# Optimization experiments

Measured on AMD Instinct MI355X. Metric: run time of the kernel, lower is better.

The kernel has to match this reference:

```python
import jax, jax.numpy as jnp
import numpy as np

N = 500000
C = 128
V = 65536


def setup_inputs() -> dict:
    key = jax.random.key(0)
    k1, k2, k3, k4 = jax.random.split(key, 4)
    feats = jax.random.normal(k1, (N, C), dtype=jnp.float32)
    W1 = jax.random.normal(k2, (C, C), dtype=jnp.float32) * (1.0 / np.sqrt(C))
    b1 = jnp.zeros((C,), dtype=jnp.float32)
    W2 = jax.random.normal(k3, (C, C), dtype=jnp.float32) * (1.0 / np.sqrt(C))
    b2 = jnp.zeros((C,), dtype=jnp.float32)
    idx = jax.random.randint(k4, (N,), 0, V, dtype=jnp.int32)
    return {"feats": feats, "W1": W1, "b1": b1, "W2": W2, "b2": b2,
            "idx": idx, "num_voxels": V}


def reference(feats, W1, b1, W2, b2, idx, num_voxels):
    # AvgPooling: per-voxel mean of point features (spvoxelize with counts)
    counts = jax.ops.segment_sum(jnp.ones((feats.shape[0],), feats.dtype), idx,
                                 num_segments=num_voxels)  # [V]
    pooled = jax.ops.segment_sum(feats, idx, num_segments=num_voxels)  # [V, C]
    pooled = pooled / jnp.clip(counts, 1.0)[:, None]
    # Upsample (nearest=True): each point gathers its voxel's pooled feature
    up = pooled[idx]  # [N, C]
    # os = x - Upsample(vs, x); os.F = mlp(os.F) * x.F; os.F = mlp2(os.F)
    os = feats - up
    h = jax.nn.relu(os @ W1 + b1) * feats
    out = jax.nn.relu(h @ W2 + b2)
    return out
```

## Files before the change

kernel.cpp:

```cpp
#include <hip/hip_runtime.h>
#include <hip/hip_fp16.h>

typedef _Float16 f16;
typedef _Float16 f16x8 __attribute__((ext_vector_type(8)));
typedef float f32x4 __attribute__((ext_vector_type(4)));

constexpr int C = 128;
constexpr int V = 65536;
constexpr int PTS = 64;
constexpr int BLOCK = 256;
constexpr int BKT = 64;

union U16 { uint4 u; f16x8 h; };

__global__ void zero_cnt(int4* __restrict__ cnt) {
    const int t = blockIdx.x * blockDim.x + threadIdx.x;
    cnt[t] = make_int4(0, 0, 0, 0);
}

__global__ void bucket_scatter(const int* __restrict__ idx, int* __restrict__ cnt,
                               int* __restrict__ bucket, int n) {
    const int t = blockIdx.x * blockDim.x + threadIdx.x;
    if (t < n) {
        const int v = idx[t];
        const int slot = atomicAdd(&cnt[v], 1);
        if (slot < BKT) bucket[(v << 6) + slot] = t;
    }
}

__global__ void __launch_bounds__(256)
pool_bucket(const float* __restrict__ feats, const int* __restrict__ bucket,
            const int* __restrict__ cnt, __half* __restrict__ pooled) {
    const int v = blockIdx.x * 4 + (threadIdx.x >> 6);
    const int lane = threadIdx.x & 63;
    const int e = min(cnt[v], BKT);
    const int* b = bucket + (v << 6);
    float ax = 0.f, ay = 0.f, bx = 0.f, by = 0.f;
    float cx = 0.f, cy = 0.f, dx = 0.f, dy = 0.f;
    int j = 0;
    for (; j + 4 <= e; j += 4) {
        const int p0 = b[j], p1 = b[j + 1], p2 = b[j + 2], p3 = b[j + 3];
        const float2 f0 = *reinterpret_cast<const float2*>(feats + (size_t)p0 * C + lane * 2);
        const float2 f1 = *reinterpret_cast<const float2*>(feats + (size_t)p1 * C + lane * 2);
        const float2 f2 = *reinterpret_cast<const float2*>(feats + (size_t)p2 * C + lane * 2);
        const float2 f3 = *reinterpret_cast<const float2*>(feats + (size_t)p3 * C + lane * 2);
        ax += f0.x; ay += f0.y; bx += f1.x; by += f1.y;
        cx += f2.x; cy += f2.y; dx += f3.x; dy += f3.y;
    }
    for (; j < e; ++j) {
        const int p0 = b[j];
        const float2 f0 = *reinterpret_cast<const float2*>(feats + (size_t)p0 * C + lane * 2);
        ax += f0.x; ay += f0.y;
    }
    const float rc = e ? 1.0f / (float)e : 0.f;
    *reinterpret_cast<__half2*>(pooled + (size_t)v * C + lane * 2) =
        __floats2half2_rn((ax + bx + cx + dx) * rc, (ay + by + cy + dy) * rc);
}

__global__ void __launch_bounds__(BLOCK)
mlp_mfma(const float* __restrict__ feats,
         const float* __restrict__ W1g,
         const float* __restrict__ b1g,
         const float* __restrict__ W2g,
         const float* __restrict__ b2g,
         const int* __restrict__ idx,
         const __half* __restrict__ pooled,
         float* __restrict__ out,
         int n) {
    __shared__ f16 osh_lds[PTS * C];
    __shared__ f16 f_lds[PTS * C];

    const int t = threadIdx.x;
    const int lane = t & 63;
    const int wv = t >> 6;
    const int l15 = lane & 15;
    const int lg = lane >> 4;
    const int chBase = 32 * wv;

    const int ch0 = chBase + l15;
    const int ch1 = chBase + 16 + l15;
    f16x8 w1f[2][4], w2f[2][4];
#pragma unroll
    for (int m = 0; m < 2; ++m) {
        const int ch = (m == 0) ? ch0 : ch1;
#pragma unroll
        for (int s = 0; s < 4; ++s) {
            f16x8 a, b;
#pragma unroll
            for (int j = 0; j < 8; ++j) {
                const int k = s * 32 + lg * 8 + j;
                a[j] = (f16)W1g[k * C + ch];
                b[j] = (f16)W2g[k * C + ch];
            }
            w1f[m][s] = a;
            w2f[m][s] = b;
        }
    }
    const float b1v[2] = {b1g[ch0], b1g[ch1]};
    const float b2v[2] = {b2g[ch0], b2g[ch1]};

    const int sp = t >> 2;
    const int sc = (t & 3) * 32;

    for (long long base = (long long)blockIdx.x * PTS; base < n;
         base += (long long)gridDim.x * PTS) {
        {
            const long long p = base + sp;
            union { float4 v[8]; float f[32]; } ff;
            union { uint4 u[4]; __half h[32]; } pl;
            if (p < n) {
#pragma unroll
                for (int j = 0; j < 8; ++j)
                    ff.v[j] = *reinterpret_cast<const float4*>(feats + (size_t)p * C + sc + j * 4);
                const int v = idx[p];
                const uint4* pp = reinterpret_cast<const uint4*>(pooled + (size_t)v * C + sc);
#pragma unroll
                for (int j = 0; j < 4; ++j) pl.u[j] = pp[j];
            } else {
#pragma unroll
                for (int j = 0; j < 8; ++j) ff.v[j] = make_float4(0.f, 0.f, 0.f, 0.f);
#pragma unroll
                for (int j = 0; j < 4; ++j) pl.u[j] = make_uint4(0, 0, 0, 0);
            }
            union { uint4 u[4]; f16 h[32]; } osv, fvh;
#pragma unroll
            for (int j = 0; j < 32; ++j) {
                const float fj = ff.f[j];
                const float mj = __half2float(pl.h[j]);
                osv.h[j] = (f16)(fj - mj);
                fvh.h[j] = (f16)fj;
            }
#pragma unroll
            for (int u = 0; u < 4; ++u) {
                const int byte = (sp * 256 + (sc + u * 8) * 2) ^ ((sp & 7) << 4);
                *reinterpret_cast<uint4*>(reinterpret_cast<char*>(osh_lds) + byte) = osv.u[u];
                *reinterpret_cast<uint4*>(reinterpret_cast<char*>(f_lds) + byte) = fvh.u[u];
            }
        }
        __syncthreads();

        f32x4 acc[2][4];
#pragma unroll
        for (int m = 0; m < 2; ++m)
#pragma unroll
            for (int q = 0; q < 4; ++q)
                acc[m][q] = (f32x4){b1v[m], b1v[m], b1v[m], b1v[m]};

#pragma unroll
        for (int s = 0; s < 4; ++s) {
            f16x8 af[4];
#pragma unroll
            for (int q = 0; q < 4; ++q) {
                const int p = q * 16 + l15;
                const int byte = (p * 256 + (s * 32 + lg * 8) * 2) ^ ((p & 7) << 4);
                U16 tmp;
                tmp.u = *reinterpret_cast<const uint4*>(reinterpret_cast<const char*>(osh_lds) + byte);
                af[q] = tmp.h;
            }
#pragma unroll
            for (int m = 0; m < 2; ++m)
#pragma unroll
                for (int q = 0; q < 4; ++q)
                    acc[m][q] = __builtin_amdgcn_mfma_f32_16x16x32_f16(af[q], w1f[m][s], acc[m][q], 0, 0, 0);
        }
        __syncthreads();

#pragma unroll
        for (int m = 0; m < 2; ++m) {
            const int ch = chBase + m * 16 + l15;
#pragma unroll
            for (int q = 0; q < 4; ++q)
#pragma unroll
                for (int r = 0; r < 4; ++r) {
                    const int d = q * 16 + lg * 4 + r;
                    const int byte = (d * 256 + ch * 2) ^ ((d & 7) << 4);
                    const float fval = (float)*reinterpret_cast<const f16*>(
                        reinterpret_cast<const char*>(f_lds) + byte);
                    const float hv = fmaxf(acc[m][q][r], 0.f) * fval;
                    *reinterpret_cast<f16*>(reinterpret_cast<char*>(osh_lds) + byte) = (f16)hv;
                }
        }
        __syncthreads();

        f32x4 acc2[2][4];
#pragma unroll
        for (int m = 0; m < 2; ++m)
#pragma unroll
            for (int q = 0; q < 4; ++q)
                acc2[m][q] = (f32x4){b2v[m], b2v[m], b2v[m], b2v[m]};

#pragma unroll
        for (int s = 0; s < 4; ++s) {
            f16x8 af[4];
#pragma unroll
            for (int q = 0; q < 4; ++q) {
                const int p = q * 16 + l15;
                const int byte = (p * 256 + (s * 32 + lg * 8) * 2) ^ ((p & 7) << 4);
                U16 tmp;
                tmp.u = *reinterpret_cast<const uint4*>(reinterpret_cast<const char*>(osh_lds) + byte);
                af[q] = tmp.h;
            }
#pragma unroll
            for (int m = 0; m < 2; ++m)
#pragma unroll
                for (int q = 0; q < 4; ++q)
                    acc2[m][q] = __builtin_amdgcn_mfma_f32_16x16x32_f16(af[q], w2f[m][s], acc2[m][q], 0, 0, 0);
        }

#pragma unroll
        for (int m = 0; m < 2; ++m) {
            const int ch = chBase + m * 16 + l15;
#pragma unroll
            for (int q = 0; q < 4; ++q)
#pragma unroll
                for (int r = 0; r < 4; ++r) {
                    const int d = q * 16 + lg * 4 + r;
                    const long long gp = base + d;
                    if (gp < n)
                        out[gp * C + ch] = fmaxf(acc2[m][q][r], 0.f);
                }
        }
        __syncthreads();
    }
}

extern "C" void kernel_launch(void* const* d_in, const int* in_sizes, int n_in,
                              void* d_out, int out_size, void* d_ws, size_t ws_size,
                              hipStream_t stream) {
    const float* feats = (const float*)d_in[0];
    const float* W1    = (const float*)d_in[1];
    const float* b1    = (const float*)d_in[2];
    const float* W2    = (const float*)d_in[3];
    const float* b2    = (const float*)d_in[4];
    const int*   idx   = (const int*)d_in[5];
    float*       out   = (float*)d_out;

    const int n = in_sizes[5];

    int* cnt    = (int*)d_ws;
    int* bucket = cnt + V;
    __half* pooled = (__half*)(bucket + (size_t)V * BKT);

    zero_cnt<<<V / (256 * 4), 256, 0, stream>>>((int4*)cnt);
    bucket_scatter<<<(n + 255) / 256, 256, 0, stream>>>(idx, cnt, bucket, n);
    pool_bucket<<<V / 4, 256, 0, stream>>>(feats, bucket, cnt, pooled);
    mlp_mfma<<<1024, BLOCK, 0, stream>>>(feats, W1, b1, W2, b2, idx,
                                         pooled, out, n);
}
```

Baseline: 235.4 us.

## Software-prefetch next tile's features, pooled rows and index into registers

Restructures the persistent loop so the global loads of feats, the gathered pooled row and the next-next index are issued right after the LDS staging barrier, overlapping them with the MFMA compute of the current tile. The index is loaded two iterations ahead to break the idx-to-pooled dependent load chain. This increases register pressure (32 floats plus 16 halves live across the GEMM), which may reduce occupancy or cause spills.

```diff
diff --git a/kernel.cpp b/kernel.cpp
--- a/kernel.cpp
+++ b/kernel.cpp
@@ -101,27 +101,34 @@
 
     const int sp = t >> 2;
     const int sc = (t & 3) * 32;
+    const long long step = (long long)gridDim.x * PTS;
+
+    union { uint4 u[8]; float f[32]; float4 v[8]; } ff;
+    union { uint4 u[4]; __half h[32]; } pl;
+    int vnx;
+    {
+        const long long p = (long long)blockIdx.x * PTS + sp;
+        if (p < n) {
+            const int v = idx[p];
+#pragma unroll
+            for (int j = 0; j < 8; ++j)
+                ff.v[j] = *reinterpret_cast<const float4*>(feats + (size_t)p * C + sc + j * 4);
+            const uint4* pp = reinterpret_cast<const uint4*>(pooled + (size_t)v * C + sc);
+#pragma unroll
+            for (int j = 0; j < 4; ++j) pl.u[j] = pp[j];
+        } else {
+#pragma unroll
+            for (int j = 0; j < 8; ++j) ff.u[j] = make_uint4(0, 0, 0, 0);
+#pragma unroll
+            for (int j = 0; j < 4; ++j) pl.u[j] = make_uint4(0, 0, 0, 0);
+        }
+        const long long p2 = p + step;
+        vnx = (p2 < n) ? idx[p2] : -1;
+    }
 
     for (long long base = (long long)blockIdx.x * PTS; base < n;
-         base += (long long)gridDim.x * PTS) {
+         base += step) {
         {
-            const long long p = base + sp;
-            union { float4 v[8]; float f[32]; } ff;
-            union { uint4 u[4]; __half h[32]; } pl;
-            if (p < n) {
-#pragma unroll
-                for (int j = 0; j < 8; ++j)
-                    ff.v[j] = *reinterpret_cast<const float4*>(feats + (size_t)p * C + sc + j * 4);
-                const int v = idx[p];
-                const uint4* pp = reinterpret_cast<const uint4*>(pooled + (size_t)v * C + sc);
-#pragma unroll
-                for (int j = 0; j < 4; ++j) pl.u[j] = pp[j];
-            } else {
-#pragma unroll
-                for (int j = 0; j < 8; ++j) ff.v[j] = make_float4(0.f, 0.f, 0.f, 0.f);
-#pragma unroll
-                for (int j = 0; j < 4; ++j) pl.u[j] = make_uint4(0, 0, 0, 0);
-            }
             union { uint4 u[4]; f16 h[32]; } osv, fvh;
 #pragma unroll
             for (int j = 0; j < 32; ++j) {
@@ -138,6 +145,28 @@
             }
         }
         __syncthreads();
+
+        {
+            const long long p = base + step + sp;
+            if (p < n) {
+#pragma unroll
+                for (int j = 0; j < 8; ++j)
+                    ff.v[j] = *reinterpret_cast<const float4*>(feats + (size_t)p * C + sc + j * 4);
+            } else {
+#pragma unroll
+                for (int j = 0; j < 8; ++j) ff.u[j] = make_uint4(0, 0, 0, 0);
+            }
+            if (vnx >= 0) {
+                const uint4* pp = reinterpret_cast<const uint4*>(pooled + (size_t)vnx * C + sc);
+#pragma unroll
+                for (int j = 0; j < 4; ++j) pl.u[j] = pp[j];
+            } else {
+#pragma unroll
+                for (int j = 0; j < 4; ++j) pl.u[j] = make_uint4(0, 0, 0, 0);
+            }
+            const long long p2 = base + 2 * step + sp;
+            vnx = (p2 < n) ? idx[p2] : -1;
+        }
 
         f32x4 acc[2][4];
 #pragma unroll
```

Result: slower. 266.9 us (+13.4%).

## Prefetch next tile via global_load_lds double staging in MLP kernel

Applied to the files above, without the earlier changes.

Moves the feats and pooled loads for the next 64-point tile into direct global-to-LDS async loads issued before the GEMMs of the current tile. This lets memory fetch overlap the MFMA work. The index for the tile after that is also prefetched into a register. Block barriers become barriers that only wait on LDS counters, so in-flight global loads are not drained at each sync. The cost is 80KB of dynamic LDS per block, which lowers occupancy, and the grid shrinks to 512 blocks.

```diff
diff --git a/kernel.cpp b/kernel.cpp
--- a/kernel.cpp
+++ b/kernel.cpp
@@ -10,8 +10,22 @@
 constexpr int PTS = 64;
 constexpr int BLOCK = 256;
 constexpr int BKT = 64;
+constexpr int MLP_GRID = 512;
+constexpr size_t MLP_LDS = 80 * 1024;
 
 union U16 { uint4 u; f16x8 h; };
+
+__device__ __forceinline__ void gll16(const void* g, void* l) {
+    auto gp = (const __attribute__((address_space(1))) unsigned int*)(unsigned long long)(uintptr_t)g;
+    auto lp = (__attribute__((address_space(3))) unsigned int*)(unsigned int)(uintptr_t)l;
+    __builtin_amdgcn_global_load_lds(gp, lp, 16, 0, 0);
+}
+
+__device__ __forceinline__ void bar_nodrain() {
+    asm volatile("s_waitcnt lgkmcnt(0)" ::: "memory");
+    __builtin_amdgcn_s_barrier();
+    asm volatile("" ::: "memory");
+}
 
 __global__ void zero_cnt(int4* __restrict__ cnt) {
     const int t = blockIdx.x * blockDim.x + threadIdx.x;
@@ -67,8 +81,11 @@
          const __half* __restrict__ pooled,
          float* __restrict__ out,
          int n) {
-    __shared__ f16 osh_lds[PTS * C];
-    __shared__ f16 f_lds[PTS * C];
+    extern __shared__ char smem[];
+    char* fstage = smem;
+    char* pstage = smem + 32768;
+    char* osh    = smem + 49152;
+    char* flds   = smem + 65536;
 
     const int t = threadIdx.x;
     const int lane = t & 63;
@@ -101,43 +118,73 @@
 
     const int sp = t >> 2;
     const int sc = (t & 3) * 32;
-
-    for (long long base = (long long)blockIdx.x * PTS; base < n;
-         base += (long long)gridDim.x * PTS) {
+    const long long step = (long long)gridDim.x * PTS;
+    const long long base0 = (long long)blockIdx.x * PTS;
+
+    int vnx;
+    {
+        const long long p = base0 + sp;
+        const long long pc = (p < n) ? p : (long long)(n - 1);
+        const int v0 = idx[pc];
+        const char* fs = (const char*)(feats + (size_t)pc * C + sc);
+#pragma unroll
+        for (int c = 0; c < 8; ++c) gll16(fs + c * 16, fstage + c * 4096 + t * 16);
+        const char* ps = (const char*)(pooled + (size_t)v0 * C + sc);
+#pragma unroll
+        for (int c = 0; c < 4; ++c) gll16(ps + c * 16, pstage + c * 4096 + t * 16);
+        const long long p1 = base0 + step + sp;
+        vnx = (p1 < n) ? idx[p1] : 0;
+    }
+
+    for (long long base = base0; base < n; base += step) {
+        asm volatile("s_waitcnt vmcnt(0)" ::: "memory");
         {
-            const long long p = base + sp;
-            union { float4 v[8]; float f[32]; } ff;
-            union { uint4 u[4]; __half h[32]; } pl;
-            if (p < n) {
-#pragma unroll
-                for (int j = 0; j < 8; ++j)
-                    ff.v[j] = *reinterpret_cast<const float4*>(feats + (size_t)p * C + sc + j * 4);
-                const int v = idx[p];
-                const uint4* pp = reinterpret_cast<const uint4*>(pooled + (size_t)v * C + sc);
-#pragma unroll
-                for (int j = 0; j < 4; ++j) pl.u[j] = pp[j];
+            const bool valid = (base + sp) < n;
+            union { uint4 u[4]; f16 h[32]; } osv, fvh;
+            if (valid) {
+#pragma unroll
+                for (int c = 0; c < 4; ++c) {
+                    union { uint4 u; float f[4]; } a, b;
+                    union { uint4 u; __half h[8]; } ph;
+                    a.u = *reinterpret_cast<const uint4*>(fstage + (2 * c) * 4096 + t * 16);
+                    b.u = *reinterpret_cast<const uint4*>(fstage + (2 * c + 1) * 4096 + t * 16);
+                    ph.u = *reinterpret_cast<const uint4*>(pstage + c * 4096 + t * 16);
+#pragma unroll
+                    for (int j = 0; j < 4; ++j) {
+                        const float f0 = a.f[j];
+                        const float f1 = b.f[j];
+                        osv.h[c * 8 + j]     = (f16)(f0 - __half2float(ph.h[j]));
+                        osv.h[c * 8 + 4 + j] = (f16)(f1 - __half2float(ph.h[4 + j]));
+                        fvh.h[c * 8 + j]     = (f16)f0;
+                        fvh.h[c * 8 + 4 + j] = (f16)f1;
+                    }
+                }
             } else {
 #pragma unroll
-                for (int j = 0; j < 8; ++j) ff.v[j] = make_float4(0.f, 0.f, 0.f, 0.f);
-#pragma unroll
-                for (int j = 0; j < 4; ++j) pl.u[j] = make_uint4(0, 0, 0, 0);
-            }
-            union { uint4 u[4]; f16 h[32]; } osv, fvh;
-#pragma unroll
-            for (int j = 0; j < 32; ++j) {
-                const float fj = ff.f[j];
-                const float mj = __half2float(pl.h[j]);
-                osv.h[j] = (f16)(fj - mj);
-                fvh.h[j] = (f16)fj;
+                for (int j = 0; j < 4; ++j) { osv.u[j] = make_uint4(0,0,0,0); fvh.u[j] = make_uint4(0,0,0,0); }
             }
 #pragma unroll
             for (int u = 0; u < 4; ++u) {
                 const int byte = (sp * 256 + (sc + u * 8) * 2) ^ ((sp & 7) << 4);
-                *reinterpret_cast<uint4*>(reinterpret_cast<char*>(osh_lds) + byte) = osv.u[u];
-                *reinterpret_cast<uint4*>(reinterpret_cast<char*>(f_lds) + byte) = fvh.u[u];
-            }
-        }
-        __syncthreads();
+                *reinterpret_cast<uint4*>(osh + byte) = osv.u[u];
+                *reinterpret_cast<uint4*>(flds + byte) = fvh.u[u];
+            }
+        }
+
+        if (base + step < n) {
+            const long long p = base + step + sp;
+            const long long pc = (p < n) ? p : (long long)(n - 1);
+            const int v = (p < n) ? vnx : 0;
+            const char* fs = (const char*)(feats + (size_t)pc * C + sc);
+#pragma unroll
+            for (int c = 0; c < 8; ++c) gll16(fs + c * 16, fstage + c * 4096 + t * 16);
+            const char* ps = (const char*)(pooled + (size_t)v * C + sc);
+#pragma unroll
+            for (int c = 0; c < 4; ++c) gll16(ps + c * 16, pstage + c * 4096 + t * 16);
+            const long long p2 = base + 2 * step + sp;
+            vnx = (p2 < n) ? idx[p2] : 0;
+        }
+        bar_nodrain();
 
         f32x4 acc[2][4];
 #pragma unroll
@@ -154,7 +201,7 @@
                 const int p = q * 16 + l15;
                 const int byte = (p * 256 + (s * 32 + lg * 8) * 2) ^ ((p & 7) << 4);
                 U16 tmp;
-                tmp.u = *reinterpret_cast<const uint4*>(reinterpret_cast<const char*>(osh_lds) + byte);
+                tmp.u = *reinterpret_cast<const uint4*>(osh + byte);
                 af[q] = tmp.h;
             }
 #pragma unroll
@@ -163,7 +210,7 @@
                 for (int q = 0; q < 4; ++q)
                     acc[m][q] = __builtin_amdgcn_mfma_f32_16x16x32_f16(af[q], w1f[m][s], acc[m][q], 0, 0, 0);
         }
-        __syncthreads();
+        bar_nodrain();
 
 #pragma unroll
         for (int m = 0; m < 2; ++m) {
@@ -174,13 +221,12 @@
                 for (int r = 0; r < 4; ++r) {
                     const int d = q * 16 + lg * 4 + r;
                     const int byte = (d * 256 + ch * 2) ^ ((d & 7) << 4);
-                    const float fval = (float)*reinterpret_cast<const f16*>(
-                        reinterpret_cast<const char*>(f_lds) + byte);
+                    const float fval = (float)*reinterpret_cast<const f16*>(flds + byte);
                     const float hv = fmaxf(acc[m][q][r], 0.f) * fval;
-                    *reinterpret_cast<f16*>(reinterpret_cast<char*>(osh_lds) + byte) = (f16)hv;
+                    *reinterpret_cast<f16*>(osh + byte) = (f16)hv;
                 }
         }
-        __syncthreads();
+        bar_nodrain();
 
         f32x4 acc2[2][4];
 #pragma unroll
@@ -197,7 +243,7 @@
                 const int p = q * 16 + l15;
                 const int byte = (p * 256 + (s * 32 + lg * 8) * 2) ^ ((p & 7) << 4);
                 U16 tmp;
-                tmp.u = *reinterpret_cast<const uint4*>(reinterpret_cast<const char*>(osh_lds) + byte);
+                tmp.u = *reinterpret_cast<const uint4*>(osh + byte);
                 af[q] = tmp.h;
             }
 #pragma unroll
@@ -220,7 +266,7 @@
                         out[gp * C + ch] = fmaxf(acc2[m][q][r], 0.f);
                 }
         }
-        __syncthreads();
+        bar_nodrain();
     }
 }
 
@@ -244,6 +290,10 @@
     zero_cnt<<<V / (256 * 4), 256, 0, stream>>>((int4*)cnt);
     bucket_scatter<<<(n + 255) / 256, 256, 0, stream>>>(idx, cnt, bucket, n);
     pool_bucket<<<V / 4, 256, 0, stream>>>(feats, bucket, cnt, pooled);
-    mlp_mfma<<<1024, BLOCK, 0, stream>>>(feats, W1, b1, W2, b2, idx,
-                                         pooled, out, n);
-}
+
+    hipFuncSetAttribute((const void*)mlp_mfma,
+                        hipFuncAttributeMaxDynamicSharedMemorySize,
+                        (int)MLP_LDS);
+    mlp_mfma<<<MLP_GRID, BLOCK, MLP_LDS, stream>>>(feats, W1, b1, W2, b2, idx,
+                                                   pooled, out, n);
+}
```

Result: slower. 243.4 us (+3.4%).

## Split MLP channels across 8 waves and double-buffer hidden activations in LDS

Applied to the files above, without the earlier changes.

The MLP kernel now runs with 512 threads per block, and each wave owns 16 output channels instead of 32. This halves the per-wave weight fragments and accumulators, cutting register pressure so more waves can hide latency. A separate h_lds buffer holds the hidden activations, which removes one barrier per tile and the trailing end-of-loop barrier. The cost is more LDS per block (48KB) and half as many blocks in the grid, which may limit how many blocks fit per CU.

```diff
diff --git a/kernel.cpp b/kernel.cpp
--- a/kernel.cpp
+++ b/kernel.cpp
@@ -8,7 +8,7 @@
 constexpr int C = 128;
 constexpr int V = 65536;
 constexpr int PTS = 64;
-constexpr int BLOCK = 256;
+constexpr int MLP_BLOCK = 512;
 constexpr int BKT = 64;
 
 union U16 { uint4 u; f16x8 h; };
@@ -57,7 +57,7 @@
         __floats2half2_rn((ax + bx + cx + dx) * rc, (ay + by + cy + dy) * rc);
 }
 
-__global__ void __launch_bounds__(BLOCK)
+__global__ void __launch_bounds__(MLP_BLOCK)
 mlp_mfma(const float* __restrict__ feats,
          const float* __restrict__ W1g,
          const float* __restrict__ b1g,
@@ -67,84 +67,76 @@
          const __half* __restrict__ pooled,
          float* __restrict__ out,
          int n) {
-    __shared__ f16 osh_lds[PTS * C];
+    __shared__ f16 os_lds[PTS * C];
     __shared__ f16 f_lds[PTS * C];
+    __shared__ f16 h_lds[PTS * C];
 
     const int t = threadIdx.x;
     const int lane = t & 63;
     const int wv = t >> 6;
     const int l15 = lane & 15;
     const int lg = lane >> 4;
-    const int chBase = 32 * wv;
-
-    const int ch0 = chBase + l15;
-    const int ch1 = chBase + 16 + l15;
-    f16x8 w1f[2][4], w2f[2][4];
-#pragma unroll
-    for (int m = 0; m < 2; ++m) {
-        const int ch = (m == 0) ? ch0 : ch1;
-#pragma unroll
-        for (int s = 0; s < 4; ++s) {
-            f16x8 a, b;
-#pragma unroll
-            for (int j = 0; j < 8; ++j) {
-                const int k = s * 32 + lg * 8 + j;
-                a[j] = (f16)W1g[k * C + ch];
-                b[j] = (f16)W2g[k * C + ch];
-            }
-            w1f[m][s] = a;
-            w2f[m][s] = b;
-        }
-    }
-    const float b1v[2] = {b1g[ch0], b1g[ch1]};
-    const float b2v[2] = {b2g[ch0], b2g[ch1]};
-
-    const int sp = t >> 2;
-    const int sc = (t & 3) * 32;
+    const int ch = 16 * wv + l15;
+
+    f16x8 w1f[4], w2f[4];
+#pragma unroll
+    for (int s = 0; s < 4; ++s) {
+        f16x8 a, b;
+#pragma unroll
+        for (int j = 0; j < 8; ++j) {
+            const int k = s * 32 + lg * 8 + j;
+            a[j] = (f16)W1g[k * C + ch];
+            b[j] = (f16)W2g[k * C + ch];
+        }
+        w1f[s] = a;
+        w2f[s] = b;
+    }
+    const float b1v = b1g[ch];
+    const float b2v = b2g[ch];
+
+    const int sp = t >> 3;
+    const int sc = (t & 7) * 16;
 
     for (long long base = (long long)blockIdx.x * PTS; base < n;
          base += (long long)gridDim.x * PTS) {
         {
             const long long p = base + sp;
-            union { float4 v[8]; float f[32]; } ff;
-            union { uint4 u[4]; __half h[32]; } pl;
+            union { float4 v4[4]; float f[16]; } ff;
+            union { uint4 u[2]; __half h[16]; } pl;
             if (p < n) {
 #pragma unroll
-                for (int j = 0; j < 8; ++j)
-                    ff.v[j] = *reinterpret_cast<const float4*>(feats + (size_t)p * C + sc + j * 4);
+                for (int j = 0; j < 4; ++j)
+                    ff.v4[j] = *reinterpret_cast<const float4*>(feats + (size_t)p * C + sc + j * 4);
                 const int v = idx[p];
                 const uint4* pp = reinterpret_cast<const uint4*>(pooled + (size_t)v * C + sc);
 #pragma unroll
-                for (int j = 0; j < 4; ++j) pl.u[j] = pp[j];
+                for (int j = 0; j < 2; ++j) pl.u[j] = pp[j];
             } else {
 #pragma unroll
-                for (int j = 0; j < 8; ++j) ff.v[j] = make_float4(0.f, 0.f, 0.f, 0.f);
-#pragma unroll
-                for (int j = 0; j < 4; ++j) pl.u[j] = make_uint4(0, 0, 0, 0);
-            }
-            union { uint4 u[4]; f16 h[32]; } osv, fvh;
-#pragma unroll
-            for (int j = 0; j < 32; ++j) {
+                for (int j = 0; j < 4; ++j) ff.v4[j] = make_float4(0.f, 0.f, 0.f, 0.f);
+#pragma unroll
+                for (int j = 0; j < 2; ++j) pl.u[j] = make_uint4(0, 0, 0, 0);
+            }
+            union { uint4 u[2]; f16 h[16]; } osv, fvh;
+#pragma unroll
+            for (int j = 0; j < 16; ++j) {
                 const float fj = ff.f[j];
-                const float mj = __half2float(pl.h[j]);
-                osv.h[j] = (f16)(fj - mj);
+                osv.h[j] = (f16)(fj - __half2float(pl.h[j]));
                 fvh.h[j] = (f16)fj;
             }
 #pragma unroll
-            for (int u = 0; u < 4; ++u) {
+            for (int u = 0; u < 2; ++u) {
                 const int byte = (sp * 256 + (sc + u * 8) * 2) ^ ((sp & 7) << 4);
-                *reinterpret_cast<uint4*>(reinterpret_cast<char*>(osh_lds) + byte) = osv.u[u];
+                *reinterpret_cast<uint4*>(reinterpret_cast<char*>(os_lds) + byte) = osv.u[u];
                 *reinterpret_cast<uint4*>(reinterpret_cast<char*>(f_lds) + byte) = fvh.u[u];
             }
         }
         __syncthreads();
 
-        f32x4 acc[2][4];
-#pragma unroll
-        for (int m = 0; m < 2; ++m)
-#pragma unroll
-            for (int q = 0; q < 4; ++q)
-                acc[m][q] = (f32x4){b1v[m], b1v[m], b1v[m], b1v[m]};
+        f32x4 acc[4];
+#pragma unroll
+        for (int q = 0; q < 4; ++q)
+            acc[q] = (f32x4){b1v, b1v, b1v, b1v};
 
 #pragma unroll
         for (int s = 0; s < 4; ++s) {
@@ -154,40 +146,31 @@
                 const int p = q * 16 + l15;
                 const int byte = (p * 256 + (s * 32 + lg * 8) * 2) ^ ((p & 7) << 4);
                 U16 tmp;
-                tmp.u = *reinterpret_cast<const uint4*>(reinterpret_cast<const char*>(osh_lds) + byte);
+                tmp.u = *reinterpret_cast<const uint4*>(reinterpret_cast<const char*>(os_lds) + byte);
                 af[q] = tmp.h;
             }
 #pragma unroll
-            for (int m = 0; m < 2; ++m)
-#pragma unroll
-                for (int q = 0; q < 4; ++q)
-                    acc[m][q] = __builtin_amdgcn_mfma_f32_16x16x32_f16(af[q], w1f[m][s], acc[m][q], 0, 0, 0);
-        }
+            for (int q = 0; q < 4; ++q)
+                acc[q] = __builtin_amdgcn_mfma_f32_16x16x32_f16(af[q], w1f[s], acc[q], 0, 0, 0);
+        }
+
+#pragma unroll
+        for (int q = 0; q < 4; ++q)
+#pragma unroll
+            for (int r = 0; r < 4; ++r) {
+                const int d = q * 16 + lg * 4 + r;
+                const int byte = (d * 256 + ch * 2) ^ ((d & 7) << 4);
+                const float fval = (float)*reinterpret_cast<const f16*>(
+                    reinterpret_cast<const char*>(f_lds) + byte);
+                const float hv = fmaxf(acc[q][r], 0.f) * fval;
+                *reinterpret_cast<f16*>(reinterpret_cast<char*>(h_lds) + byte) = (f16)hv;
+            }
         __syncthreads();
 
-#pragma unroll
-        for (int m = 0; m < 2; ++m) {
-            const int ch = chBase + m * 16 + l15;
-#pragma unroll
-            for (int q = 0; q < 4; ++q)
-#pragma unroll
-                for (int r = 0; r < 4; ++r) {
-                    const int d = q * 16 + lg * 4 + r;
-                    const int byte = (d * 256 + ch * 2) ^ ((d & 7) << 4);
-                    const float fval = (float)*reinterpret_cast<const f16*>(
-                        reinterpret_cast<const char*>(f_lds) + byte);
-                    const float hv = fmaxf(acc[m][q][r], 0.f) * fval;
-                    *reinterpret_cast<f16*>(reinterpret_cast<char*>(osh_lds) + byte) = (f16)hv;
-                }
-        }
-        __syncthreads();
-
-        f32x4 acc2[2][4];
-#pragma unroll
-        for (int m = 0; m < 2; ++m)
-#pragma unroll
-            for (int q = 0; q < 4; ++q)
-                acc2[m][q] = (f32x4){b2v[m], b2v[m], b2v[m], b2v[m]};
+        f32x4 acc2[4];
+#pragma unroll
+        for (int q = 0; q < 4; ++q)
+            acc2[q] = (f32x4){b2v, b2v, b2v, b2v};
 
 #pragma unroll
         for (int s = 0; s < 4; ++s) {
@@ -197,30 +180,23 @@
                 const int p = q * 16 + l15;
                 const int byte = (p * 256 + (s * 32 + lg * 8) * 2) ^ ((p & 7) << 4);
                 U16 tmp;
-                tmp.u = *reinterpret_cast<const uint4*>(reinterpret_cast<const char*>(osh_lds) + byte);
+                tmp.u = *reinterpret_cast<const uint4*>(reinterpret_cast<const char*>(h_lds) + byte);
                 af[q] = tmp.h;
             }
 #pragma unroll
-            for (int m = 0; m < 2; ++m)
-#pragma unroll
-                for (int q = 0; q < 4; ++q)
-                    acc2[m][q] = __builtin_amdgcn_mfma_f32_16x16x32_f16(af[q], w2f[m][s], acc2[m][q], 0, 0, 0);
-        }
-
-#pragma unroll
-        for (int m = 0; m < 2; ++m) {
-            const int ch = chBase + m * 16 + l15;
-#pragma unroll
             for (int q = 0; q < 4; ++q)
-#pragma unroll
-                for (int r = 0; r < 4; ++r) {
-                    const int d = q * 16 + lg * 4 + r;
-                    const long long gp = base + d;
-                    if (gp < n)
-                        out[gp * C + ch] = fmaxf(acc2[m][q][r], 0.f);
-                }
-        }
-        __syncthreads();
+                acc2[q] = __builtin_amdgcn_mfma_f32_16x16x32_f16(af[q], w2f[s], acc2[q], 0, 0, 0);
+        }
+
+#pragma unroll
+        for (int q = 0; q < 4; ++q)
+#pragma unroll
+            for (int r = 0; r < 4; ++r) {
+                const int d = q * 16 + lg * 4 + r;
+                const long long gp = base + d;
+                if (gp < n)
+                    out[gp * C + ch] = fmaxf(acc2[q][r], 0.f);
+            }
     }
 }
 
@@ -244,6 +220,6 @@
     zero_cnt<<<V / (256 * 4), 256, 0, stream>>>((int4*)cnt);
     bucket_scatter<<<(n + 255) / 256, 256, 0, stream>>>(idx, cnt, bucket, n);
     pool_bucket<<<V / 4, 256, 0, stream>>>(feats, bucket, cnt, pooled);
-    mlp_mfma<<<1024, BLOCK, 0, stream>>>(feats, W1, b1, W2, b2, idx,
-                                         pooled, out, n);
-}
+    mlp_mfma<<<512, MLP_BLOCK, 0, stream>>>(feats, W1, b1, W2, b2, idx,
+                                            pooled, out, n);
+}
```

Measured after the change: 207.0 us. 12.1% less time.
